# Kernel optimization log

Hardware: AMD Instinct MI355X
Metric: run time of the kernel (lower is better)

The kernel has to match this reference:

```python
import jax, jax.numpy as jnp
import numpy as np

B, T, C = 4, 2048, 1024
NH = 16
HD = C // NH  # 64


def setup_inputs() -> dict:
    key = jax.random.key(0)
    k1, k2, k3, k4, k5 = jax.random.split(key, 5)
    s_in = 1.0 / np.sqrt(C)
    return {
        "x": jax.random.normal(k1, (B, T, C), dtype=jnp.float32),
        "attention_mask": jnp.ones((B, T), dtype=jnp.float32),
        "W_qkv": jax.random.normal(k2, (C, 3 * C), dtype=jnp.float32) * s_in,
        "b_qkv": jnp.zeros((3 * C,), dtype=jnp.float32),
        "W_out": jax.random.normal(k3, (C, C), dtype=jnp.float32) * s_in,
        "b_out": jnp.zeros((C,), dtype=jnp.float32),
    }


def reference(x, attention_mask, W_qkv, b_qkv, W_out, b_out):
    Bx, Tx, Cx = x.shape
    # QKV projection: (B,T,3C)
    qkv = x @ W_qkv + b_qkv
    Q, K, V = jnp.split(qkv, 3, axis=-1)
    # (B, NH, T, HD)
    Q = Q.reshape(Bx, Tx, NH, HD).transpose(0, 2, 1, 3)
    K = K.reshape(Bx, Tx, NH, HD).transpose(0, 2, 1, 3)
    V = V.reshape(Bx, Tx, NH, HD).transpose(0, 2, 1, 3)
    # scaled scores (B, NH, T, T)
    scores = jnp.einsum("bhqd,bhkd->bhqk", Q, K) * (1.0 / np.sqrt(HD))
    # causal mask: set strictly-upper triangle to -inf (mask-fill semantics)
    causal = jnp.tril(jnp.ones((Tx, Tx), dtype=bool))[None, None]
    scores = jnp.where(causal, scores, -jnp.inf)
    # additive padding mask
    pad = (1.0 - attention_mask)[:, None, None, :] * jnp.finfo(scores.dtype).min
    scores = scores + pad
    attn = jax.nn.softmax(scores, axis=-1)
    # weighted values -> (B, T, C)
    wv = jnp.einsum("bhqk,bhkd->bhqd", attn, V)
    wv = wv.transpose(0, 2, 1, 3).reshape(Bx, Tx, Cx)
    return wv @ W_out + b_out
```

## Files before the change

kernel.cpp:

```cpp
#include <hip/hip_runtime.h>
#include <math.h>

constexpr int BB = 4;
constexpr int TT = 2048;
constexpr int CC = 1024;
constexpr int NHH = 16;
constexpr int HDD = 64;
constexpr int C3 = 3 * CC;

typedef __bf16 bf16x8 __attribute__((ext_vector_type(8)));
typedef __bf16 bf16x4 __attribute__((ext_vector_type(4)));
typedef float  f32x4  __attribute__((ext_vector_type(4)));

__device__ __forceinline__ unsigned short f2bf(float x) {
    union { float f; unsigned u; } v; v.f = x;
    unsigned r = v.u + 0x7fffu + ((v.u >> 16) & 1u);
    return (unsigned short)(r >> 16);
}

#define AS1(p) ((const __attribute__((address_space(1))) void*)(p))
#define AS3(p) ((__attribute__((address_space(3))) void*)(p))

constexpr float SM2 = 17.312340490667561f;

constexpr int CAST_BLOCKS = (BB * TT * CC / 4) / 256;
constexpr int TQKV_BLOCKS = (C3 / 64) * (CC / 64);
constexpr int TOUT_BLOCKS = (CC / 64) * (CC / 64);
constexpr int KB_BLOCKS   = (BB * TT) / 256;

__global__ __launch_bounds__(256) void prep(
    const float* __restrict__ x,
    const float* __restrict__ Wqkv,
    const float* __restrict__ Wout,
    const float* __restrict__ amask,
    unsigned short* __restrict__ xb,
    unsigned short* __restrict__ Wqkvt,
    unsigned short* __restrict__ Woutt,
    float* __restrict__ kbias)
{
    __shared__ float tile[64][65];
    const int bid = blockIdx.x;
    const int t = threadIdx.x;

    if (bid < CAST_BLOCKS) {
        const int i = bid * 256 + t;
        float4 v = ((const float4*)x)[i];
        ushort4 o;
        o.x = f2bf(v.x); o.y = f2bf(v.y); o.z = f2bf(v.z); o.w = f2bf(v.w);
        ((ushort4*)xb)[i] = o;
        return;
    }
    if (bid >= CAST_BLOCKS + TQKV_BLOCKS + TOUT_BLOCKS) {
        const int i = (bid - CAST_BLOCKS - TQKV_BLOCKS - TOUT_BLOCKS) * 256 + t;
        kbias[i] = (amask[i] - 1.0f) * 1.0e38f - SM2;
        return;
    }

    const float* src; unsigned short* dst; int R, Cn, r0, c0;
    if (bid < CAST_BLOCKS + TQKV_BLOCKS) {
        const int tb = bid - CAST_BLOCKS;
        src = Wqkv; dst = Wqkvt; R = CC; Cn = C3;
        c0 = (tb % (C3 / 64)) * 64; r0 = (tb / (C3 / 64)) * 64;
    } else {
        const int tb = bid - CAST_BLOCKS - TQKV_BLOCKS;
        src = Wout; dst = Woutt; R = CC; Cn = CC;
        c0 = (tb % (CC / 64)) * 64; r0 = (tb / (CC / 64)) * 64;
    }

    const int lr = t >> 4, lc = (t & 15) * 4;
    #pragma unroll
    for (int s = 0; s < 4; ++s) {
        float4 v = *(const float4*)&src[(size_t)(r0 + lr + s * 16) * Cn + c0 + lc];
        tile[lr + s * 16][lc + 0] = v.x;
        tile[lr + s * 16][lc + 1] = v.y;
        tile[lr + s * 16][lc + 2] = v.z;
        tile[lr + s * 16][lc + 3] = v.w;
    }
    __syncthreads();
    const int oi = t >> 2, oc = (t & 3) * 16;
    unsigned short buf[16];
    #pragma unroll
    for (int u = 0; u < 16; ++u)
        buf[u] = f2bf(tile[oc + u][oi]);
    unsigned short* d = &dst[(size_t)(c0 + oi) * R + r0 + oc];
    *(uint4*)(d + 0) = *(uint4*)&buf[0];
    *(uint4*)(d + 8) = *(uint4*)&buf[8];
}

template<bool VSPLIT>
__global__ __launch_bounds__(256, 2) void gemm_bt_mfma(
    const unsigned short* __restrict__ A,
    const unsigned short* __restrict__ Bt,
    const float* __restrict__ bias,
    float* __restrict__ OutF,
    unsigned short* __restrict__ Qp,
    unsigned short* __restrict__ Kp,
    unsigned short* __restrict__ Vtp,
    int M, int N, int K, float qscale)
{
    __shared__ alignas(16) unsigned short As[2][128 * 64];
    __shared__ alignas(16) unsigned short Bs[2][128 * 64];

    const int tid  = threadIdx.x;
    const int w    = tid >> 6;
    const int lane = tid & 63;
    const int quad = lane >> 4;
    const int col  = lane & 15;

    const int nX  = gridDim.x;
    const int lin = blockIdx.y * nX + blockIdx.x;
    const int pos = lin >> 3;
    const int mt  = ((lin & 7) << 3) | (pos & 7);
    const int nt  = pos >> 3;
    const int m0 = mt * 128, n0 = nt * 128;
    const int wr = w >> 1, wc = w & 1;

    f32x4 acc[4][4];
    #pragma unroll
    for (int i = 0; i < 4; ++i)
        #pragma unroll
        for (int j = 0; j < 4; ++j)
            #pragma unroll
            for (int r = 0; r < 4; ++r)
                acc[i][j][r] = 0.0f;

    const int srow = tid >> 3;
    const int spos = tid & 7;
    char* AsB = (char*)&As[0][0];
    char* BsB = (char*)&Bs[0][0];

    const int nk = K >> 6;

    auto DMA = [&](int kt, int buf) {
        const int k0 = kt << 6;
        #pragma unroll
        for (int i = 0; i < 4; ++i) {
            const int row = srow + 32 * i;
            const int sc = spos ^ (row & 7);
            __builtin_amdgcn_global_load_lds(
                AS1(A + (size_t)(m0 + row) * K + k0 + sc * 8),
                AS3(AsB + buf * 16384 + i * 4096 + w * 1024), 16, 0, 0);
            __builtin_amdgcn_global_load_lds(
                AS1(Bt + (size_t)(n0 + row) * K + k0 + sc * 8),
                AS3(BsB + buf * 16384 + i * 4096 + w * 1024), 16, 0, 0);
        }
    };

    DMA(0, 0);
    DMA(1, 1);
    asm volatile("s_waitcnt vmcnt(8)" ::: "memory");
    __builtin_amdgcn_s_barrier();

    for (int kt = 0; kt < nk; ++kt) {
        const int cur = kt & 1;
        const unsigned short* as = &As[cur][0];
        const unsigned short* bs = &Bs[cur][0];

        #pragma unroll
        for (int ks = 0; ks < 2; ++ks) {
            bf16x8 af[4], bf[4];
            #pragma unroll
            for (int i = 0; i < 4; ++i) {
                const int ra = wr * 64 + i * 16 + col;
                const int pa = ((quad + ks * 4) ^ (ra & 7)) * 8;
                af[i] = *(const bf16x8*)&as[ra * 64 + pa];
                const int rb = wc * 64 + i * 16 + col;
                const int pb = ((quad + ks * 4) ^ (rb & 7)) * 8;
                bf[i] = *(const bf16x8*)&bs[rb * 64 + pb];
            }
            #pragma unroll
            for (int i = 0; i < 4; ++i)
                #pragma unroll
                for (int j = 0; j < 4; ++j)
                    acc[i][j] = __builtin_amdgcn_mfma_f32_16x16x32_bf16(af[i], bf[j], acc[i][j], 0, 0, 0);
        }

        __builtin_amdgcn_s_barrier();
        if (kt + 2 < nk) {
            DMA(kt + 2, cur);
            asm volatile("s_waitcnt vmcnt(8)" ::: "memory");
        } else {
            asm volatile("s_waitcnt vmcnt(0)" ::: "memory");
        }
        __builtin_amdgcn_s_barrier();
    }

    if (VSPLIT) {
        if (n0 < CC) {
            #pragma unroll
            for (int i = 0; i < 4; ++i)
                #pragma unroll
                for (int r = 0; r < 4; ++r) {
                    const int m = m0 + wr * 64 + i * 16 + quad * 4 + r;
                    #pragma unroll
                    for (int j = 0; j < 4; ++j) {
                        const int n = n0 + wc * 64 + j * 16 + col;
                        Qp[(size_t)m * CC + n] = f2bf((acc[i][j][r] + bias[n]) * qscale);
                    }
                }
        } else if (n0 < 2 * CC) {
            #pragma unroll
            for (int i = 0; i < 4; ++i) {
                const int mb   = m0 + wr * 64 + i * 16 + quad * 4;
                const int bidx = mb >> 11;
                const int tloc = mb & 2047;
                #pragma unroll
                for (int j = 0; j < 4; ++j) {
                    const int n  = n0 + wc * 64 + j * 16 + col;
                    const int hh = (n - CC) >> 6;
                    const int dd = (n - CC) & 63;
                    #pragma unroll
                    for (int r = 0; r < 4; ++r)
                        Kp[(((size_t)bidx * NHH + hh) * TT + tloc + r) * HDD + dd] =
                            f2bf(acc[i][j][r] + bias[n]);
                }
            }
        } else {
            #pragma unroll
            for (int i = 0; i < 4; ++i) {
                const int mb   = m0 + wr * 64 + i * 16 + quad * 4;
                const int bidx = mb >> 11;
                const int tloc = mb & 2047;
                const int ktile = tloc >> 6, tc = tloc & 63;
                #pragma unroll
                for (int j = 0; j < 4; ++j) {
                    const int n  = n0 + wc * 64 + j * 16 + col;
                    const int hh = (n - 2 * CC) >> 6;
                    const int dd = (n - 2 * CC) & 63;
                    unsigned short pk[4];
                    #pragma unroll
                    for (int r = 0; r < 4; ++r)
                        pk[r] = f2bf(acc[i][j][r] + bias[n]);
                    *(uint2*)&Vtp[((((size_t)bidx * NHH + hh) * 32 + ktile) * HDD + dd) * 64 + tc] =
                        *(const uint2*)pk;
                }
            }
        }
    } else {
        #pragma unroll
        for (int i = 0; i < 4; ++i)
            #pragma unroll
            for (int r = 0; r < 4; ++r) {
                const int m = m0 + wr * 64 + i * 16 + quad * 4 + r;
                #pragma unroll
                for (int j = 0; j < 4; ++j) {
                    const int n = n0 + wc * 64 + j * 16 + col;
                    OutF[(size_t)m * N + n] = acc[i][j][r] + bias[n];
                }
            }
    }
}

constexpr int PP = 72;

__global__ __launch_bounds__(256, 3) void attn_mfma(
    const unsigned short* __restrict__ Qp,
    const unsigned short* __restrict__ Kp,
    const unsigned short* __restrict__ Vtp,
    const float* __restrict__ kbias,
    unsigned short* __restrict__ WV)
{
    __shared__ alignas(16) unsigned short Ks [2][64 * 64];
    __shared__ alignas(16) unsigned short Vts[2][64 * 64];
    __shared__ alignas(16) __bf16        Ps[4][32 * PP];

    const int tid  = threadIdx.x;
    const int w    = tid >> 6;
    const int lane = tid & 63;
    const int quad = lane >> 4;
    const int col  = lane & 15;

    const int gi = blockIdx.x;
    const int j  = gi >> 3;
    const int bh = ((gi & 7) << 3) | (j & 7);
    const int qb = 15 - (j >> 3);
    const int b = bh >> 4, h = bh & 15;

    const unsigned short* Qg = Qp + (size_t)b * TT * CC + (size_t)h * HDD;
    const unsigned short* Kg = Kp + (size_t)bh * TT * HDD;
    const unsigned short* Vg = Vtp + (size_t)bh * 32 * HDD * 64;
    const float* kb_g = kbias + b * TT;

    const int srow = tid >> 3;
    const int sch  = (tid & 7) ^ (srow & 7);
    char* KsB  = (char*)&Ks[0][0];
    char* VtsB = (char*)&Vts[0][0];

    const int qw = qb * 128 + w * 32;
    const int ntiles = 2 * qb + 2;

    bf16x8 qfa0 = *(const bf16x8*)(Qg + (size_t)(qw + col) * CC + quad * 8);
    bf16x8 qfa1 = *(const bf16x8*)(Qg + (size_t)(qw + col) * CC + 32 + quad * 8);
    bf16x8 qfb0 = *(const bf16x8*)(Qg + (size_t)(qw + 16 + col) * CC + quad * 8);
    bf16x8 qfb1 = *(const bf16x8*)(Qg + (size_t)(qw + 16 + col) * CC + 32 + quad * 8);

    f32x4 o[2][4];
    float l[2] = {0.0f, 0.0f};
    #pragma unroll
    for (int hh = 0; hh < 2; ++hh)
        #pragma unroll
        for (int t = 0; t < 4; ++t)
            #pragma unroll
            for (int r = 0; r < 4; ++r) o[hh][t][r] = 0.0f;

    auto DMA = [&](int tile, int buf) {
        #pragma unroll
        for (int i = 0; i < 2; ++i) {
            __builtin_amdgcn_global_load_lds(
                AS1(Kg + (size_t)(tile * 64 + srow + 32 * i) * HDD + sch * 8),
                AS3(KsB + buf * 8192 + i * 4096 + w * 1024), 16, 0, 0);
            __builtin_amdgcn_global_load_lds(
                AS1(Vg + ((size_t)tile * 64 + srow + 32 * i) * 64 + sch * 8),
                AS3(VtsB + buf * 8192 + i * 4096 + w * 1024), 16, 0, 0);
        }
    };

    f32x4 kbc[4], kbn[4];
    DMA(0, 0);
    #pragma unroll
    for (int t = 0; t < 4; ++t)
        kbc[t] = *(const f32x4*)&kb_g[t * 16 + quad * 4];
    DMA(1, 1);
    #pragma unroll
    for (int t = 0; t < 4; ++t)
        kbn[t] = *(const f32x4*)&kb_g[64 + t * 16 + quad * 4];
    asm volatile("s_waitcnt vmcnt(8)" ::: "memory");
    __builtin_amdgcn_s_barrier();

    for (int it = 0; it < ntiles; ++it) {
        const int kt  = it << 6;
        const int cur = it & 1;

        if (kt <= qw + 31) {
            const unsigned short* ksb = &Ks[cur][0];
            const unsigned short* vsb = &Vts[cur][0];

            f32x4 s[2][4];
            __builtin_amdgcn_s_setprio(1);
            #pragma unroll
            for (int t = 0; t < 4; ++t) {
                const int row = t * 16 + col;
                const int c0 = (quad ^ (row & 7)) * 8;
                const int c1 = ((quad + 4) ^ (row & 7)) * 8;
                bf16x8 k0 = *(const bf16x8*)&ksb[row * 64 + c0];
                bf16x8 k1 = *(const bf16x8*)&ksb[row * 64 + c1];
                f32x4 za = __builtin_amdgcn_mfma_f32_16x16x32_bf16(k0, qfa0, kbc[t], 0, 0, 0);
                za = __builtin_amdgcn_mfma_f32_16x16x32_bf16(k1, qfa1, za, 0, 0, 0);
                s[0][t] = za;
                f32x4 zb = __builtin_amdgcn_mfma_f32_16x16x32_bf16(k0, qfb0, kbc[t], 0, 0, 0);
                zb = __builtin_amdgcn_mfma_f32_16x16x32_bf16(k1, qfb1, zb, 0, 0, 0);
                s[1][t] = zb;
            }
            __builtin_amdgcn_s_setprio(0);

            if (kt + 64 > qw) {
                #pragma unroll
                for (int hh = 0; hh < 2; ++hh) {
                    const int q = qw + hh * 16 + col;
                    #pragma unroll
                    for (int t = 0; t < 4; ++t) {
                        float pv[4];
                        #pragma unroll
                        for (int r = 0; r < 4; ++r) {
                            const int key = kt + t * 16 + quad * 4 + r;
                            float p = __builtin_amdgcn_exp2f(s[hh][t][r]);
                            if (key > q) p = 0.0f;
                            l[hh] += p;
                            pv[r] = p;
                        }
                        bf16x4 pk4 = { (__bf16)pv[0], (__bf16)pv[1],
                                       (__bf16)pv[2], (__bf16)pv[3] };
                        *(bf16x4*)&Ps[w][(hh * 16 + col) * PP + t * 16 + quad * 4] = pk4;
                    }
                }
            } else {
                #pragma unroll
                for (int hh = 0; hh < 2; ++hh) {
                    #pragma unroll
                    for (int t = 0; t < 4; ++t) {
                        float pv[4];
                        #pragma unroll
                        for (int r = 0; r < 4; ++r) {
                            float p = __builtin_amdgcn_exp2f(s[hh][t][r]);
                            l[hh] += p;
                            pv[r] = p;
                        }
                        bf16x4 pk4 = { (__bf16)pv[0], (__bf16)pv[1],
                                       (__bf16)pv[2], (__bf16)pv[3] };
                        *(bf16x4*)&Ps[w][(hh * 16 + col) * PP + t * 16 + quad * 4] = pk4;
                    }
                }
            }

            bf16x8 pa0 = *(const bf16x8*)&Ps[w][col * PP + quad * 8];
            bf16x8 pa1 = *(const bf16x8*)&Ps[w][col * PP + 32 + quad * 8];
            bf16x8 pb0 = *(const bf16x8*)&Ps[w][(16 + col) * PP + quad * 8];
            bf16x8 pb1 = *(const bf16x8*)&Ps[w][(16 + col) * PP + 32 + quad * 8];
            __builtin_amdgcn_s_setprio(1);
            #pragma unroll
            for (int t = 0; t < 4; ++t) {
                const int row = t * 16 + col;
                const int c0 = (quad ^ (row & 7)) * 8;
                const int c1 = ((quad + 4) ^ (row & 7)) * 8;
                bf16x8 v0 = *(const bf16x8*)&vsb[row * 64 + c0];
                bf16x8 v1 = *(const bf16x8*)&vsb[row * 64 + c1];
                o[0][t] = __builtin_amdgcn_mfma_f32_16x16x32_bf16(pa0, v0, o[0][t], 0, 0, 0);
                o[0][t] = __builtin_amdgcn_mfma_f32_16x16x32_bf16(pa1, v1, o[0][t], 0, 0, 0);
                o[1][t] = __builtin_amdgcn_mfma_f32_16x16x32_bf16(pb0, v0, o[1][t], 0, 0, 0);
                o[1][t] = __builtin_amdgcn_mfma_f32_16x16x32_bf16(pb1, v1, o[1][t], 0, 0, 0);
            }
            __builtin_amdgcn_s_setprio(0);
        }

        __builtin_amdgcn_s_barrier();

        #pragma unroll
        for (int t = 0; t < 4; ++t) kbc[t] = kbn[t];

        if (it + 2 < ntiles) {
            DMA(it + 2, cur);
            #pragma unroll
            for (int t = 0; t < 4; ++t)
                kbn[t] = *(const f32x4*)&kb_g[(it + 2) * 64 + t * 16 + quad * 4];
            asm volatile("s_waitcnt vmcnt(8)" ::: "memory");
        } else {
            asm volatile("s_waitcnt vmcnt(0)" ::: "memory");
        }
        __builtin_amdgcn_s_barrier();
    }

    #pragma unroll
    for (int hh = 0; hh < 2; ++hh) {
        l[hh] += __shfl_xor(l[hh], 16);
        l[hh] += __shfl_xor(l[hh], 32);
    }
    #pragma unroll
    for (int hh = 0; hh < 2; ++hh) {
        #pragma unroll
        for (int r = 0; r < 4; ++r) {
            const float Lr = __shfl(l[hh], (lane & 48) | (quad * 4 + r));
            const float inv = 1.0f / Lr;
            const int q = qw + hh * 16 + quad * 4 + r;
            unsigned short* dst = WV + ((size_t)b * TT + q) * CC + (size_t)h * HDD;
            #pragma unroll
            for (int t = 0; t < 4; ++t)
                dst[t * 16 + col] = f2bf(o[hh][t][r] * inv);
        }
    }
}

extern "C" void kernel_launch(void* const* d_in, const int* in_sizes, int n_in,
                              void* d_out, int out_size, void* d_ws, size_t ws_size,
                              hipStream_t stream) {
    const float* x     = (const float*)d_in[0];
    const float* amask = (const float*)d_in[1];
    const float* Wqkv  = (const float*)d_in[2];
    const float* bqkv  = (const float*)d_in[3];
    const float* Wout  = (const float*)d_in[4];
    const float* bout  = (const float*)d_in[5];
    float* out = (float*)d_out;

    const int M = BB * TT;

    unsigned short* xb    = (unsigned short*)d_ws;
    unsigned short* Wqkvt = xb    + (size_t)M * CC;
    unsigned short* Woutt = Wqkvt + (size_t)C3 * CC;
    unsigned short* Qp    = Woutt + (size_t)CC * CC;
    unsigned short* Kp    = Qp    + (size_t)M * CC;
    unsigned short* Vtp   = Kp    + (size_t)M * CC;
    unsigned short* wvb   = Vtp   + (size_t)M * CC;
    float*          kbias = (float*)(wvb + (size_t)M * CC);

    dim3 blk(256);

    prep<<<dim3(CAST_BLOCKS + TQKV_BLOCKS + TOUT_BLOCKS + KB_BLOCKS), blk, 0, stream>>>(
        x, Wqkv, Wout, amask, xb, Wqkvt, Woutt, kbias);

    gemm_bt_mfma<true><<<dim3(C3 / 128, M / 128), blk, 0, stream>>>(
        xb, Wqkvt, bqkv, nullptr, Qp, Kp, Vtp, M, C3, CC, 0.18033688011112043f);
    attn_mfma<<<dim3(1024), dim3(256), 0, stream>>>(
        Qp, Kp, Vtp, kbias, wvb);
    gemm_bt_mfma<false><<<dim3(CC / 128, M / 128), blk, 0, stream>>>(
        wvb, Woutt, bout, out, nullptr, nullptr, nullptr, M, CC, CC, 1.0f);
}
```

Before: 230.4 us.

## Replace QKV GEMM with 256x256-tile, 8-wave kernel with interleaved prefetch

Adds a dedicated QKV projection kernel that uses 256x256 output tiles with 512 threads (8 waves) instead of 128x128 tiles with 256 threads. Next-tile DMA loads are issued in slices between the MFMA phases, and the MFMA phases are wrapped in s_setprio. Blocks are mapped to XCDs for L2 locality. The larger tile raises arithmetic intensity and cuts global traffic, at the cost of 128 KB of LDS per block and heavy register pressure, which may limit occupancy to one block per CU.

```diff
diff --git a/kernel.cpp b/kernel.cpp
--- a/kernel.cpp
+++ b/kernel.cpp
@@ -22,6 +22,7 @@
 #define AS3(p) ((__attribute__((address_space(3))) void*)(p))
 
 constexpr float SM2 = 17.312340490667561f;
+constexpr float QSCALE = 0.18033688011112043f;
 
 constexpr int CAST_BLOCKS = (BB * TT * CC / 4) / 256;
 constexpr int TQKV_BLOCKS = (C3 / 64) * (CC / 64);
@@ -87,16 +88,192 @@
     *(uint4*)(d + 8) = *(uint4*)&buf[8];
 }
 
-template<bool VSPLIT>
-__global__ __launch_bounds__(256, 2) void gemm_bt_mfma(
+__global__ __launch_bounds__(512, 2) void gemm_qkv8(
+    const unsigned short* __restrict__ A,
+    const unsigned short* __restrict__ Bt,
+    const float* __restrict__ bias,
+    unsigned short* __restrict__ Qp,
+    unsigned short* __restrict__ Kp,
+    unsigned short* __restrict__ Vtp)
+{
+    __shared__ alignas(16) unsigned short As[2][256 * 64];
+    __shared__ alignas(16) unsigned short Bs[2][256 * 64];
+
+    const int tid  = threadIdx.x;
+    const int w    = tid >> 6;
+    const int lane = tid & 63;
+    const int quad = lane >> 4;
+    const int col  = lane & 15;
+    const int wr = w >> 2, wc = w & 3;
+
+    const int lin = blockIdx.x;
+    const int xcd = lin & 7, idx = lin >> 3;
+    const int mt  = xcd * 4 + (idx & 3);
+    const int nt  = idx >> 2;
+    const int m0 = mt * 256, n0 = nt * 256;
+
+    f32x4 acc[8][4];
+    #pragma unroll
+    for (int i = 0; i < 8; ++i)
+        #pragma unroll
+        for (int j = 0; j < 4; ++j)
+            #pragma unroll
+            for (int r = 0; r < 4; ++r)
+                acc[i][j][r] = 0.0f;
+
+    const int srow = tid >> 3;
+    const int sch  = (tid & 7) ^ (srow & 7);
+    char* AsB = (char*)&As[0][0];
+    char* BsB = (char*)&Bs[0][0];
+
+    constexpr int K  = CC;
+    constexpr int nk = K / 64;
+
+    auto ISSUE = [&](int t, int slot, int u) {
+        const int k0 = t << 6;
+        if (u < 4) {
+            __builtin_amdgcn_global_load_lds(
+                AS1(A + (size_t)(m0 + u * 64 + srow) * K + k0 + sch * 8),
+                AS3(AsB + slot * 32768 + u * 8192 + w * 1024), 16, 0, 0);
+        } else {
+            const int v = u - 4;
+            __builtin_amdgcn_global_load_lds(
+                AS1(Bt + (size_t)(n0 + v * 64 + srow) * K + k0 + sch * 8),
+                AS3(BsB + slot * 32768 + v * 8192 + w * 1024), 16, 0, 0);
+        }
+    };
+
+    auto LDA = [&](const unsigned short* as, int ih, bf16x8* dst) {
+        #pragma unroll
+        for (int i = 0; i < 4; ++i)
+            #pragma unroll
+            for (int ks = 0; ks < 2; ++ks) {
+                const int ra = wr * 128 + (ih * 4 + i) * 16 + col;
+                dst[i * 2 + ks] = *(const bf16x8*)&as[ra * 64 + ((quad + ks * 4) ^ (ra & 7)) * 8];
+            }
+    };
+    auto LDB = [&](const unsigned short* bs, int jh, bf16x8* dst) {
+        #pragma unroll
+        for (int j = 0; j < 2; ++j)
+            #pragma unroll
+            for (int ks = 0; ks < 2; ++ks) {
+                const int rb = wc * 64 + (jh * 2 + j) * 16 + col;
+                dst[j * 2 + ks] = *(const bf16x8*)&bs[rb * 64 + ((quad + ks * 4) ^ (rb & 7)) * 8];
+            }
+    };
+    auto MM = [&](int ih, int jh, const bf16x8* af, const bf16x8* bf) {
+        #pragma unroll
+        for (int i = 0; i < 4; ++i)
+            #pragma unroll
+            for (int j = 0; j < 2; ++j)
+                #pragma unroll
+                for (int ks = 0; ks < 2; ++ks)
+                    acc[ih * 4 + i][jh * 2 + j] = __builtin_amdgcn_mfma_f32_16x16x32_bf16(
+                        af[i * 2 + ks], bf[j * 2 + ks], acc[ih * 4 + i][jh * 2 + j], 0, 0, 0);
+    };
+
+    #pragma unroll
+    for (int u = 0; u < 8; ++u) ISSUE(0, 0, u);
+    asm volatile("s_waitcnt vmcnt(0)" ::: "memory");
+    __builtin_amdgcn_s_barrier();
+
+    for (int t = 0; t < nk; ++t) {
+        const int c = t & 1;
+        const unsigned short* as = &As[c][0];
+        const unsigned short* bs = &Bs[c][0];
+        const bool pf = (t + 1 < nk);
+        bf16x8 af[8], bf0[4], bf1[4];
+
+        LDA(as, 0, af);
+        LDB(bs, 0, bf0);
+        if (pf) { ISSUE(t + 1, c ^ 1, 0); ISSUE(t + 1, c ^ 1, 1); ISSUE(t + 1, c ^ 1, 2); }
+        __builtin_amdgcn_s_barrier();
+        __builtin_amdgcn_s_setprio(1);
+        MM(0, 0, af, bf0);
+        __builtin_amdgcn_s_setprio(0);
+        __builtin_amdgcn_s_barrier();
+
+        LDB(bs, 1, bf1);
+        if (pf) { ISSUE(t + 1, c ^ 1, 3); ISSUE(t + 1, c ^ 1, 4); ISSUE(t + 1, c ^ 1, 5); }
+        __builtin_amdgcn_s_barrier();
+        __builtin_amdgcn_s_setprio(1);
+        MM(0, 1, af, bf1);
+        __builtin_amdgcn_s_setprio(0);
+        __builtin_amdgcn_s_barrier();
+
+        LDA(as, 1, af);
+        if (pf) { ISSUE(t + 1, c ^ 1, 6); ISSUE(t + 1, c ^ 1, 7); }
+        __builtin_amdgcn_s_barrier();
+        __builtin_amdgcn_s_setprio(1);
+        MM(1, 0, af, bf0);
+        __builtin_amdgcn_s_setprio(0);
+        __builtin_amdgcn_s_barrier();
+
+        __builtin_amdgcn_s_setprio(1);
+        MM(1, 1, af, bf1);
+        __builtin_amdgcn_s_setprio(0);
+        asm volatile("s_waitcnt vmcnt(0)" ::: "memory");
+        __builtin_amdgcn_s_barrier();
+    }
+
+    if (n0 < CC) {
+        #pragma unroll
+        for (int i = 0; i < 8; ++i)
+            #pragma unroll
+            for (int r = 0; r < 4; ++r) {
+                const int m = m0 + wr * 128 + i * 16 + quad * 4 + r;
+                #pragma unroll
+                for (int j = 0; j < 4; ++j) {
+                    const int n = n0 + wc * 64 + j * 16 + col;
+                    Qp[(size_t)m * CC + n] = f2bf((acc[i][j][r] + bias[n]) * QSCALE);
+                }
+            }
+    } else if (n0 < 2 * CC) {
+        #pragma unroll
+        for (int i = 0; i < 8; ++i) {
+            const int mb   = m0 + wr * 128 + i * 16 + quad * 4;
+            const int bidx = mb >> 11;
+            const int tloc = mb & 2047;
+            #pragma unroll
+            for (int j = 0; j < 4; ++j) {
+                const int n  = n0 + wc * 64 + j * 16 + col;
+                const int hh = (n - CC) >> 6;
+                const int dd = (n - CC) & 63;
+                #pragma unroll
+                for (int r = 0; r < 4; ++r)
+                    Kp[(((size_t)bidx * NHH + hh) * TT + tloc + r) * HDD + dd] =
+                        f2bf(acc[i][j][r] + bias[n]);
+            }
+        }
+    } else {
+        #pragma unroll
+        for (int i = 0; i < 8; ++i) {
+            const int mb   = m0 + wr * 128 + i * 16 + quad * 4;
+            const int bidx = mb >> 11;
+            const int tloc = mb & 2047;
+            const int ktile = tloc >> 6, tc = tloc & 63;
+            #pragma unroll
+            for (int j = 0; j < 4; ++j) {
+                const int n  = n0 + wc * 64 + j * 16 + col;
+                const int hh = (n - 2 * CC) >> 6;
+                const int dd = (n - 2 * CC) & 63;
+                unsigned short pk[4];
+                #pragma unroll
+                for (int r = 0; r < 4; ++r)
+                    pk[r] = f2bf(acc[i][j][r] + bias[n]);
+                *(uint2*)&Vtp[((((size_t)bidx * NHH + hh) * 32 + ktile) * HDD + dd) * 64 + tc] =
+                    *(const uint2*)pk;
+            }
+        }
+    }
+}
+
+__global__ __launch_bounds__(256, 2) void gemm_out(
     const unsigned short* __restrict__ A,
     const unsigned short* __restrict__ Bt,
     const float* __restrict__ bias,
     float* __restrict__ OutF,
-    unsigned short* __restrict__ Qp,
-    unsigned short* __restrict__ Kp,
-    unsigned short* __restrict__ Vtp,
-    int M, int N, int K, float qscale)
+    int M, int N, int K)
 {
     __shared__ alignas(16) unsigned short As[2][128 * 64];
     __shared__ alignas(16) unsigned short Bs[2][128 * 64];
@@ -185,70 +362,17 @@
         __builtin_amdgcn_s_barrier();
     }
 
-    if (VSPLIT) {
-        if (n0 < CC) {
-            #pragma unroll
-            for (int i = 0; i < 4; ++i)
-                #pragma unroll
-                for (int r = 0; r < 4; ++r) {
-                    const int m = m0 + wr * 64 + i * 16 + quad * 4 + r;
-                    #pragma unroll
-                    for (int j = 0; j < 4; ++j) {
-                        const int n = n0 + wc * 64 + j * 16 + col;
-                        Qp[(size_t)m * CC + n] = f2bf((acc[i][j][r] + bias[n]) * qscale);
-                    }
-                }
-        } else if (n0 < 2 * CC) {
-            #pragma unroll
-            for (int i = 0; i < 4; ++i) {
-                const int mb   = m0 + wr * 64 + i * 16 + quad * 4;
-                const int bidx = mb >> 11;
-                const int tloc = mb & 2047;
-                #pragma unroll
-                for (int j = 0; j < 4; ++j) {
-                    const int n  = n0 + wc * 64 + j * 16 + col;
-                    const int hh = (n - CC) >> 6;
-                    const int dd = (n - CC) & 63;
-                    #pragma unroll
-                    for (int r = 0; r < 4; ++r)
-                        Kp[(((size_t)bidx * NHH + hh) * TT + tloc + r) * HDD + dd] =
-                            f2bf(acc[i][j][r] + bias[n]);
-                }
-            }
-        } else {
-            #pragma unroll
-            for (int i = 0; i < 4; ++i) {
-                const int mb   = m0 + wr * 64 + i * 16 + quad * 4;
-                const int bidx = mb >> 11;
-                const int tloc = mb & 2047;
-                const int ktile = tloc >> 6, tc = tloc & 63;
-                #pragma unroll
-                for (int j = 0; j < 4; ++j) {
-                    const int n  = n0 + wc * 64 + j * 16 + col;
-                    const int hh = (n - 2 * CC) >> 6;
-                    const int dd = (n - 2 * CC) & 63;
-                    unsigned short pk[4];
-                    #pragma unroll
-                    for (int r = 0; r < 4; ++r)
-                        pk[r] = f2bf(acc[i][j][r] + bias[n]);
-                    *(uint2*)&Vtp[((((size_t)bidx * NHH + hh) * 32 + ktile) * HDD + dd) * 64 + tc] =
-                        *(const uint2*)pk;
-                }
-            }
-        }
-    } else {
-        #pragma unroll
-        for (int i = 0; i < 4; ++i)
-            #pragma unroll
-            for (int r = 0; r < 4; ++r) {
-                const int m = m0 + wr * 64 + i * 16 + quad * 4 + r;
-                #pragma unroll
-                for (int j = 0; j < 4; ++j) {
-                    const int n = n0 + wc * 64 + j * 16 + col;
-                    OutF[(size_t)m * N + n] = acc[i][j][r] + bias[n];
-                }
-            }
-    }
+    #pragma unroll
+    for (int i = 0; i < 4; ++i)
+        #pragma unroll
+        for (int r = 0; r < 4; ++r) {
+            const int m = m0 + wr * 64 + i * 16 + quad * 4 + r;
+            #pragma unroll
+            for (int j = 0; j < 4; ++j) {
+                const int n = n0 + wc * 64 + j * 16 + col;
+                OutF[(size_t)m * N + n] = acc[i][j][r] + bias[n];
+            }
+        }
 }
 
 constexpr int PP = 72;
@@ -476,10 +600,10 @@
     prep<<<dim3(CAST_BLOCKS + TQKV_BLOCKS + TOUT_BLOCKS + KB_BLOCKS), blk, 0, stream>>>(
         x, Wqkv, Wout, amask, xb, Wqkvt, Woutt, kbias);
 
-    gemm_bt_mfma<true><<<dim3(C3 / 128, M / 128), blk, 0, stream>>>(
-        xb, Wqkvt, bqkv, nullptr, Qp, Kp, Vtp, M, C3, CC, 0.18033688011112043f);
+    gemm_qkv8<<<dim3(384), dim3(512), 0, stream>>>(
+        xb, Wqkvt, bqkv, Qp, Kp, Vtp);
     attn_mfma<<<dim3(1024), dim3(256), 0, stream>>>(
         Qp, Kp, Vtp, kbias, wvb);
-    gemm_bt_mfma<false><<<dim3(CC / 128, M / 128), blk, 0, stream>>>(
-        wvb, Woutt, bout, out, nullptr, nullptr, nullptr, M, CC, CC, 1.0f);
+    gemm_out<<<dim3(CC / 128, M / 128), blk, 0, stream>>>(
+        wvb, Woutt, bout, out, M, CC, CC);
 }
```

Measured after the change: 243.6 us. 1.06x slower.
